# Performance work log

Measured on AMD Instinct MI355X. Metric: run time of the kernel, lower is better.

## Reference

```python
import jax, jax.numpy as jnp
import numpy as np
import math

D_MODEL = 1024
N_HEADS = 8
D_FF = 4 * D_MODEL
EPS = 1e-5


def layer_norm(x, g, b):
    mu = jnp.mean(x, axis=-1, keepdims=True)
    var = jnp.mean(jnp.square(x - mu), axis=-1, keepdims=True)
    return (x - mu) / jnp.sqrt(var + EPS) * g + b


def setup_inputs() -> dict:
    key = jax.random.key(0)
    ks = jax.random.split(key, 8)
    B, S = 1, 4096
    x = jax.random.normal(ks[0], (B, S, D_MODEL), dtype=jnp.float32)
    # linear params (stored as [in, out]); init scale ~ 1/sqrt(fan_in)
    qkv_w = jax.random.normal(ks[1], (D_MODEL, 3 * D_MODEL), dtype=jnp.float32) * (1.0 / math.sqrt(D_MODEL))
    qkv_b = jnp.zeros((3 * D_MODEL,), dtype=jnp.float32)
    w1 = jax.random.normal(ks[2], (D_MODEL, D_FF), dtype=jnp.float32) * (1.0 / math.sqrt(D_MODEL))
    b1 = jnp.zeros((D_FF,), dtype=jnp.float32)
    w2 = jax.random.normal(ks[3], (D_FF, D_MODEL), dtype=jnp.float32) * (1.0 / math.sqrt(D_FF))
    b2 = jnp.zeros((D_MODEL,), dtype=jnp.float32)
    ln1_g = jnp.ones((D_MODEL,), dtype=jnp.float32)
    ln1_b = jnp.zeros((D_MODEL,), dtype=jnp.float32)
    ln2_g = jnp.ones((D_MODEL,), dtype=jnp.float32)
    ln2_b = jnp.zeros((D_MODEL,), dtype=jnp.float32)
    return {"x": x, "ln1_g": ln1_g, "ln1_b": ln1_b, "qkv_w": qkv_w, "qkv_b": qkv_b,
            "ln2_g": ln2_g, "ln2_b": ln2_b, "w1": w1, "b1": b1, "w2": w2, "b2": b2}


def reference(x, ln1_g, ln1_b, qkv_w, qkv_b, ln2_g, ln2_b, w1, b1, w2, b2):
    B, S, D = x.shape
    hd = D // N_HEADS
    scaler = math.sqrt(hd)

    h = layer_norm(x, ln1_g, ln1_b)                       # [B,S,D]
    qkv = h @ qkv_w + qkv_b                               # [B,S,3D]
    q, k, v = jnp.split(qkv, 3, axis=-1)
    # b s (h d) -> b h s d
    def split_heads(t):
        return t.reshape(B, S, N_HEADS, hd).transpose(0, 2, 1, 3)
    q, k, v = split_heads(q), split_heads(k), split_heads(v)
    scores = jnp.einsum('bhqd,bhkd->bhqk', q, k) / scaler  # [B,H,S,S] materialized, as in source
    attn = jax.nn.softmax(scores, axis=-1)
    heads = jnp.einsum('bhqk,bhkd->bhqd', attn, v)        # [B,H,S,hd]
    attn_score = heads.transpose(0, 2, 1, 3).reshape(B, S, D)  # b h t d -> b t (h d)
    # NOTE: source returns attn_score (the proj Linear output is discarded)
    h = attn_score + h                                     # residual with ln1 output
    h = layer_norm(h, ln2_g, ln2_b)
    h = jax.nn.gelu(h @ w1 + b1, approximate=False) @ w2 + b2  # no final residual
    return h
```

## Files before the change

### kernel.cpp

```cpp
#include <hip/hip_runtime.h>
#include <stdint.h>


typedef __bf16 bf16;
typedef __attribute__((ext_vector_type(8))) __bf16 bf16x8;
typedef __attribute__((ext_vector_type(4))) __bf16 bf16x4;
typedef __attribute__((ext_vector_type(4))) float f32x4;

#define DEV static __device__ __forceinline__

#define QSCALE 0.12751741687f

DEV void gload_lds16(const void* gsrc, void* ldst) {
  typedef const __attribute__((address_space(1))) uint32_t gq_t;
  typedef __attribute__((address_space(3))) uint32_t lq_t;
  __builtin_amdgcn_global_load_lds((gq_t*)(uintptr_t)gsrc, (lq_t*)(uintptr_t)ldst,
                                   16, 0, 0);
}

DEV f32x4 mfma16(bf16x8 a, bf16x8 b, f32x4 c) {
  return __builtin_amdgcn_mfma_f32_16x16x32_bf16(a, b, c, 0, 0, 0);
}

__global__ __launch_bounds__(256) void ln1_kernel(
    const float* __restrict__ x, const float* __restrict__ gw,
    const float* __restrict__ bw, bf16* __restrict__ out) {
  int row = blockIdx.x, t = threadIdx.x;
  const float* xr = x + (size_t)row * 1024;
  f32x4 v = *(const f32x4*)(xr + t * 4);
  float s = v[0] + v[1] + v[2] + v[3];
  float s2 = v[0] * v[0] + v[1] * v[1] + v[2] * v[2] + v[3] * v[3];
#pragma unroll
  for (int off = 1; off < 64; off <<= 1) {
    s += __shfl_xor(s, off);
    s2 += __shfl_xor(s2, off);
  }
  __shared__ float red[8];
  if ((t & 63) == 0) { red[t >> 6] = s; red[4 + (t >> 6)] = s2; }
  __syncthreads();
  s = red[0] + red[1] + red[2] + red[3];
  s2 = red[4] + red[5] + red[6] + red[7];
  float mu = s * (1.f / 1024.f);
  float rstd = rsqrtf(s2 * (1.f / 1024.f) - mu * mu + 1e-5f);
  f32x4 gv = *(const f32x4*)(gw + t * 4);
  f32x4 bv = *(const f32x4*)(bw + t * 4);
  bf16x4 o;
#pragma unroll
  for (int j = 0; j < 4; j++) o[j] = (bf16)((v[j] - mu) * rstd * gv[j] + bv[j]);
  *(bf16x4*)(out + (size_t)row * 1024 + t * 4) = o;
}

__global__ __launch_bounds__(256) void resid_ln2_kernel(
    const bf16* __restrict__ Op, const float* __restrict__ lbuf,
    const bf16* __restrict__ h, const float* __restrict__ gw,
    const float* __restrict__ bw, bf16* __restrict__ out) {
  int row = blockIdx.x, t = threadIdx.x;
  int head = t >> 5;
  float l = 0.f;
  float acc[4] = {0.f, 0.f, 0.f, 0.f};
#pragma unroll
  for (int z = 0; z < 4; z++) {
    l += lbuf[(size_t)(z * 8 + head) * 4096 + row];
    bf16x4 ov = *(const bf16x4*)(Op + (size_t)z * 4096 * 1024 +
                                 (size_t)row * 1024 + t * 4);
#pragma unroll
    for (int j = 0; j < 4; j++) acc[j] += (float)ov[j];
  }
  float rl = 1.0f / l;
  bf16x4 hv = *(const bf16x4*)(h + (size_t)row * 1024 + t * 4);
  float vv[4];
#pragma unroll
  for (int j = 0; j < 4; j++) vv[j] = acc[j] * rl + (float)hv[j];
  float s = vv[0] + vv[1] + vv[2] + vv[3];
  float s2 = vv[0] * vv[0] + vv[1] * vv[1] + vv[2] * vv[2] + vv[3] * vv[3];
#pragma unroll
  for (int off = 1; off < 64; off <<= 1) {
    s += __shfl_xor(s, off);
    s2 += __shfl_xor(s2, off);
  }
  __shared__ float red[8];
  if ((t & 63) == 0) { red[t >> 6] = s; red[4 + (t >> 6)] = s2; }
  __syncthreads();
  s = red[0] + red[1] + red[2] + red[3];
  s2 = red[4] + red[5] + red[6] + red[7];
  float mu = s * (1.f / 1024.f);
  float rstd = rsqrtf(s2 * (1.f / 1024.f) - mu * mu + 1e-5f);
  f32x4 gv = *(const f32x4*)(gw + t * 4);
  f32x4 bv = *(const f32x4*)(bw + t * 4);
  bf16x4 o;
#pragma unroll
  for (int j = 0; j < 4; j++) o[j] = (bf16)((vv[j] - mu) * rstd * gv[j] + bv[j]);
  *(bf16x4*)(out + (size_t)row * 1024 + t * 4) = o;
}

__global__ __launch_bounds__(256) void transpose_f32_bf16(
    const float* __restrict__ in, bf16* __restrict__ out, int R, int C) {
  __shared__ float tile[32][33];
  int c0 = blockIdx.x * 32, r0 = blockIdx.y * 32;
  int tx = threadIdx.x & 31, ty = threadIdx.x >> 5;
#pragma unroll
  for (int j = 0; j < 4; j++)
    tile[ty + 8 * j][tx] = in[(size_t)(r0 + ty + 8 * j) * C + c0 + tx];
  __syncthreads();
#pragma unroll
  for (int j = 0; j < 4; j++)
    out[(size_t)(c0 + ty + 8 * j) * R + r0 + tx] = (bf16)tile[tx][ty + 8 * j];
}

template <int EPILOG>
__global__ __launch_bounds__(512) void gemm8_kernel(
    const bf16* __restrict__ A, const bf16* __restrict__ Bt,
    const float* __restrict__ bias, bf16* __restrict__ Cout,
    bf16* __restrict__ Vout, int M, int N, int K) {
  __shared__ bf16 sA[256 * 64];
  __shared__ bf16 sB[128 * 64];
  int nwg = gridDim.x * gridDim.y;
  int bid = blockIdx.y * gridDim.x + blockIdx.x;
  int swz = (bid & 7) * (nwg >> 3) + (bid >> 3);
  int bx = swz % gridDim.x, by = swz / gridDim.x;
  int m0 = by * 256, n0 = bx * 128;
  int tid = threadIdx.x;
  int wave = tid >> 6, lane = tid & 63;
  int lr = lane & 15, lg = lane >> 4;
  int wr = (wave >> 1) * 64, wc = (wave & 1) * 64;

  f32x4 acc[4][4] = {};

  int srow = tid >> 3;
  int scol = (tid & 7) * 8;
  const bf16* Abase = A + (size_t)(m0 + srow) * K + scol;
  const bf16* Bbase = Bt + (size_t)(n0 + srow) * K + scol;

  for (int kt = 0; kt < K; kt += 64) {
#pragma unroll
    for (int i = 0; i < 4; i++)
      gload_lds16(Abase + (size_t)(i * 64) * K + kt,
                  (char*)sA + i * 8192 + wave * 1024);
#pragma unroll
    for (int i = 0; i < 2; i++)
      gload_lds16(Bbase + (size_t)(i * 64) * K + kt,
                  (char*)sB + i * 8192 + wave * 1024);
    __syncthreads();
    bf16x8 af[4][2], bfv[4][2];
#pragma unroll
    for (int m = 0; m < 4; m++)
#pragma unroll
      for (int kk = 0; kk < 2; kk++)
        af[m][kk] = *(const bf16x8*)&sA[(wr + m * 16 + lr) * 64 + kk * 32 + lg * 8];
#pragma unroll
    for (int n = 0; n < 4; n++)
#pragma unroll
      for (int kk = 0; kk < 2; kk++)
        bfv[n][kk] = *(const bf16x8*)&sB[(wc + n * 16 + lr) * 64 + kk * 32 + lg * 8];
#pragma unroll
    for (int kk = 0; kk < 2; kk++)
#pragma unroll
      for (int m = 0; m < 4; m++)
#pragma unroll
        for (int n = 0; n < 4; n++)
          acc[m][n] = mfma16(af[m][kk], bfv[n][kk], acc[m][n]);
    __syncthreads();
  }

#pragma unroll
  for (int n = 0; n < 4; n++) {
    int col = n0 + wc + n * 16 + lr;
    float bs = bias[col];
#pragma unroll
    for (int m = 0; m < 4; m++) {
      int row0 = m0 + wr + m * 16 + lg * 4;
      if constexpr (EPILOG == 3) {
        if (col >= 2048) {
          bf16x4 pk;
#pragma unroll
          for (int r = 0; r < 4; r++) pk[r] = (bf16)(acc[m][n][r] + bs);
          *(bf16x4*)(Vout + (size_t)(col - 2048) * 4096 + row0) = pk;
          continue;
        }
      }
#pragma unroll
      for (int r = 0; r < 4; r++) {
        float v = acc[m][n][r] + bs;
        if constexpr (EPILOG == 1) {
          float u = v + 0.044715f * v * v * v;
          float e = __builtin_amdgcn_exp2f(-2.3021144f * u);
          v = v / (1.0f + e);
        }
        if constexpr (EPILOG == 3) { if (col < 1024) v *= QSCALE; }
        Cout[(size_t)(row0 + r) * N + col] = (bf16)v;
      }
    }
  }
}

__global__ __launch_bounds__(256) void gemm_ffn2_kernel(
    const bf16* __restrict__ A, const bf16* __restrict__ Bt,
    const float* __restrict__ bias, float* __restrict__ Cout,
    int M, int N, int K) {
  __shared__ bf16 sA[64 * 64];
  __shared__ bf16 sB[128 * 64];
  int nwg = gridDim.x * gridDim.y;
  int bid = blockIdx.y * gridDim.x + blockIdx.x;
  int swz = (bid & 7) * (nwg >> 3) + (bid >> 3);
  int bx = swz % gridDim.x, by = swz / gridDim.x;
  int m0 = by * 64, n0 = bx * 128;
  int tid = threadIdx.x;
  int wave = tid >> 6, lane = tid & 63;
  int lr = lane & 15, lg = lane >> 4;
  int wr = (wave >> 1) * 32, wc = (wave & 1) * 64;

  f32x4 acc[2][4] = {};

  int srow = tid >> 3;
  int scol = (tid & 7) * 8;
  const bf16* Abase = A + (size_t)(m0 + srow) * K + scol;
  const bf16* Bbase = Bt + (size_t)(n0 + srow) * K + scol;

  for (int kt = 0; kt < K; kt += 64) {
#pragma unroll
    for (int i = 0; i < 2; i++)
      gload_lds16(Abase + (size_t)(i * 32) * K + kt,
                  (char*)sA + i * 4096 + wave * 1024);
#pragma unroll
    for (int i = 0; i < 4; i++)
      gload_lds16(Bbase + (size_t)(i * 32) * K + kt,
                  (char*)sB + i * 4096 + wave * 1024);
    __syncthreads();
    bf16x8 af[2][2], bfv[4][2];
#pragma unroll
    for (int m = 0; m < 2; m++)
#pragma unroll
      for (int kk = 0; kk < 2; kk++)
        af[m][kk] = *(const bf16x8*)&sA[(wr + m * 16 + lr) * 64 + kk * 32 + lg * 8];
#pragma unroll
    for (int n = 0; n < 4; n++)
#pragma unroll
      for (int kk = 0; kk < 2; kk++)
        bfv[n][kk] = *(const bf16x8*)&sB[(wc + n * 16 + lr) * 64 + kk * 32 + lg * 8];
#pragma unroll
    for (int kk = 0; kk < 2; kk++)
#pragma unroll
      for (int m = 0; m < 2; m++)
#pragma unroll
        for (int n = 0; n < 4; n++)
          acc[m][n] = mfma16(af[m][kk], bfv[n][kk], acc[m][n]);
    __syncthreads();
  }

#pragma unroll
  for (int n = 0; n < 4; n++) {
    int col = n0 + wc + n * 16 + lr;
    float bs = bias[col];
#pragma unroll
    for (int m = 0; m < 2; m++) {
#pragma unroll
      for (int r = 0; r < 4; r++) {
        int row = m0 + wr + m * 16 + lg * 4 + r;
        Cout[(size_t)row * N + col] = acc[m][n][r] + bs;
      }
    }
  }
}

__global__ __launch_bounds__(256) void attn_kernel(
    const bf16* __restrict__ qkv, const bf16* __restrict__ vt,
    bf16* __restrict__ opart, float* __restrict__ lbuf) {
  constexpr int S = 4096, C3 = 3072;
  __shared__ bf16 sK[64 * 128];
  __shared__ bf16 sV[128 * 64];
  __shared__ bf16 sP[4 * 32 * 64];
  int hh = blockIdx.y;
  int q0 = blockIdx.x * 128;
  int z = blockIdx.z;
  int kv_begin = z * (S / 4), kv_end = kv_begin + (S / 4);
  bf16* obuf = opart + (size_t)z * 4096 * 1024;
  int tid = threadIdx.x, wave = tid >> 6, lane = tid & 63;
  int lr = lane & 15, lg = lane >> 4;

  bf16x8 qf[2][4];
#pragma unroll
  for (int qs = 0; qs < 2; qs++) {
    const bf16* qrow =
        qkv + (size_t)(q0 + wave * 32 + qs * 16 + lr) * C3 + hh * 128 + lg * 8;
#pragma unroll
    for (int kk = 0; kk < 4; kk++) qf[qs][kk] = *(const bf16x8*)(qrow + kk * 32);
  }
  f32x4 o[2][8] = {};
  float lsum[2] = {0.f, 0.f};

  const int krow_s = tid >> 4;
  const int kcb = (tid & 15) * 16;
  const int scbK = kcb ^ ((krow_s & 7) << 4);
  const int vrow_s = tid >> 3;
  const int vcb = (tid & 7) * 16;
  const int scbV = vcb ^ ((vrow_s & 7) << 4);

  const bf16* kbase = qkv + 1024 + hh * 128 + scbK / 2;
  const bf16* vbase = vt + (size_t)(hh * 128 + vrow_s) * S + scbV / 2;

  for (int kv0 = kv_begin; kv0 < kv_end; kv0 += 64) {
#pragma unroll
    for (int i = 0; i < 4; i++)
      gload_lds16(kbase + (size_t)(kv0 + i * 16 + krow_s) * C3,
                  (char*)sK + i * 4096 + wave * 1024);
#pragma unroll
    for (int i = 0; i < 4; i++)
      gload_lds16(vbase + (size_t)(i * 32) * S + kv0,
                  (char*)sV + i * 4096 + wave * 1024);
    __syncthreads();

    char* pw = (char*)sP + wave * 4096;

#pragma unroll
    for (int nf = 0; nf < 4; nf++) {
      f32x4 sc0 = {0.f, 0.f, 0.f, 0.f}, sc1 = sc0;
      __builtin_amdgcn_s_setprio(1);
#pragma unroll
      for (int kk = 0; kk < 4; kk++) {
        int krow = nf * 16 + lr;
        int db = (kk * 64 + lg * 16) ^ ((krow & 7) << 4);
        bf16x8 kf = *(const bf16x8*)((const char*)sK + krow * 256 + db);
        sc0 = mfma16(kf, qf[0][kk], sc0);
        sc1 = mfma16(kf, qf[1][kk], sc1);
      }
      __builtin_amdgcn_s_setprio(0);
      f32x4 scs[2] = {sc0, sc1};
#pragma unroll
      for (int qs = 0; qs < 2; qs++) {
        float p0 = __builtin_amdgcn_exp2f(scs[qs][0]);
        float p1 = __builtin_amdgcn_exp2f(scs[qs][1]);
        float p2 = __builtin_amdgcn_exp2f(scs[qs][2]);
        float p3 = __builtin_amdgcn_exp2f(scs[qs][3]);
        lsum[qs] += (p0 + p1) + (p2 + p3);
        bf16x4 pk;
        pk[0] = (bf16)p0; pk[1] = (bf16)p1; pk[2] = (bf16)p2; pk[3] = (bf16)p3;
        *(bf16x4*)(pw + (qs * 16 + lr) * 128 +
                   ((nf * 32 + lg * 8) ^ ((lr & 7) << 4))) = pk;
      }
    }

    bf16x8 pa[2][2];
#pragma unroll
    for (int qs = 0; qs < 2; qs++)
#pragma unroll
      for (int kk = 0; kk < 2; kk++) {
        int db = (kk * 64 + lg * 16) ^ ((lr & 7) << 4);
        pa[qs][kk] = *(const bf16x8*)(pw + (qs * 16 + lr) * 128 + db);
      }
    __builtin_amdgcn_s_setprio(1);
#pragma unroll
    for (int df = 0; df < 8; df++) {
#pragma unroll
      for (int kk = 0; kk < 2; kk++) {
        int vrow = df * 16 + lr;
        int db = (kk * 64 + lg * 16) ^ ((vrow & 7) << 4);
        bf16x8 vf = *(const bf16x8*)((const char*)sV + vrow * 128 + db);
        o[0][df] = mfma16(pa[0][kk], vf, o[0][df]);
        o[1][df] = mfma16(pa[1][kk], vf, o[1][df]);
      }
    }
    __builtin_amdgcn_s_setprio(0);
    __syncthreads();
  }

#pragma unroll
  for (int qs = 0; qs < 2; qs++) {
    float ls = lsum[qs];
    ls += __shfl_xor(ls, 16);
    ls += __shfl_xor(ls, 32);
    if (lg == 0)
      lbuf[(size_t)(z * 8 + hh) * 4096 + q0 + wave * 32 + qs * 16 + lr] = ls;
#pragma unroll
    for (int df = 0; df < 8; df++) {
      int col = hh * 128 + df * 16 + lr;
#pragma unroll
      for (int r = 0; r < 4; r++) {
        int row = q0 + wave * 32 + qs * 16 + lg * 4 + r;
        obuf[(size_t)row * 1024 + col] = (bf16)o[qs][df][r];
      }
    }
  }
}

extern "C" void kernel_launch(void* const* d_in, const int* in_sizes, int n_in,
                              void* d_out, int out_size, void* d_ws, size_t ws_size,
                              hipStream_t stream) {
  const float* x     = (const float*)d_in[0];
  const float* ln1_g = (const float*)d_in[1];
  const float* ln1_b = (const float*)d_in[2];
  const float* qkv_w = (const float*)d_in[3];
  const float* qkv_b = (const float*)d_in[4];
  const float* ln2_g = (const float*)d_in[5];
  const float* ln2_b = (const float*)d_in[6];
  const float* w1    = (const float*)d_in[7];
  const float* b1    = (const float*)d_in[8];
  const float* w2    = (const float*)d_in[9];
  const float* b2    = (const float*)d_in[10];

  char* ws = (char*)d_ws;
  const size_t MB = 1ull << 20;
  bf16*  h    = (bf16*)(ws + 0);
  bf16*  qkv  = (bf16*)(ws + 8 * MB);
  bf16*  h2   = (bf16*)(ws + 8 * MB);
  bf16*  w1T  = (bf16*)(ws + 16 * MB);
  bf16*  w2T  = (bf16*)(ws + 24 * MB);
  bf16*  vt   = (bf16*)(ws + 32 * MB);
  bf16*  Op   = (bf16*)(ws + 40 * MB);
  bf16*  ffn1 = (bf16*)(ws + 40 * MB);
  float* lbuf = (float*)(ws + 72 * MB);
  bf16*  wTq  = (bf16*)(ws + 72 * MB + 512 * 1024);
  float* outp = (float*)d_out;

  ln1_kernel<<<4096, 256, 0, stream>>>(x, ln1_g, ln1_b, h);
  transpose_f32_bf16<<<dim3(3072 / 32, 1024 / 32), 256, 0, stream>>>(qkv_w, wTq, 1024, 3072);
  gemm8_kernel<3><<<dim3(3072 / 128, 4096 / 256), 512, 0, stream>>>(
      h, wTq, qkv_b, qkv, vt, 4096, 3072, 1024);
  attn_kernel<<<dim3(32, 8, 4), 256, 0, stream>>>(qkv, vt, Op, lbuf);
  transpose_f32_bf16<<<dim3(4096 / 32, 1024 / 32), 256, 0, stream>>>(w1, w1T, 1024, 4096);
  transpose_f32_bf16<<<dim3(1024 / 32, 4096 / 32), 256, 0, stream>>>(w2, w2T, 4096, 1024);
  resid_ln2_kernel<<<4096, 256, 0, stream>>>(Op, lbuf, h, ln2_g, ln2_b, h2);
  gemm8_kernel<1><<<dim3(4096 / 128, 4096 / 256), 512, 0, stream>>>(
      h2, w1T, b1, ffn1, nullptr, 4096, 4096, 1024);
  gemm_ffn2_kernel<<<dim3(1024 / 128, 4096 / 64), 256, 0, stream>>>(
      ffn1, w2T, b2, outp, 4096, 1024, 4096);
}
```

Before: 277.3 us.

## Rewrite QKV/FFN1 GEMM as 256x256 double-buffered pipelined kernel with swizzled LDS

Replaces the 256x128 single-buffered GEMM with a 256x256 tile kernel that double-buffers A and B in 128KB of dynamic LDS. It interleaves quarter-tile async loads with MFMA quadrants using fine-grained barriers and vmcnt waits, and uses XOR-swizzled LDS addressing to avoid bank conflicts. The aim is to hide global load latency behind compute and raise arithmetic intensity per block. In exchange, the grid gets fewer, larger blocks (192 for QKV, 256 for FFN1) and each block holds 128 accumulator registers per lane, which may hurt occupancy and load balance across 256 CUs.

```diff
diff --git a/kernel.cpp b/kernel.cpp
--- a/kernel.cpp
+++ b/kernel.cpp
@@ -108,58 +108,112 @@
 }
 
 template <int EPILOG>
-__global__ __launch_bounds__(512) void gemm8_kernel(
+__global__ __launch_bounds__(512) void gemm8p_kernel(
     const bf16* __restrict__ A, const bf16* __restrict__ Bt,
     const float* __restrict__ bias, bf16* __restrict__ Cout,
     bf16* __restrict__ Vout, int M, int N, int K) {
-  __shared__ bf16 sA[256 * 64];
-  __shared__ bf16 sB[128 * 64];
+  extern __shared__ char smem[];
   int nwg = gridDim.x * gridDim.y;
   int bid = blockIdx.y * gridDim.x + blockIdx.x;
   int swz = (bid & 7) * (nwg >> 3) + (bid >> 3);
   int bx = swz % gridDim.x, by = swz / gridDim.x;
-  int m0 = by * 256, n0 = bx * 128;
-  int tid = threadIdx.x;
-  int wave = tid >> 6, lane = tid & 63;
+  int m0 = by * 256, n0 = bx * 256;
+  int tid = threadIdx.x, wave = tid >> 6, lane = tid & 63;
   int lr = lane & 15, lg = lane >> 4;
-  int wr = (wave >> 1) * 64, wc = (wave & 1) * 64;
-
-  f32x4 acc[4][4] = {};
-
-  int srow = tid >> 3;
-  int scol = (tid & 7) * 8;
-  const bf16* Abase = A + (size_t)(m0 + srow) * K + scol;
-  const bf16* Bbase = Bt + (size_t)(n0 + srow) * K + scol;
-
-  for (int kt = 0; kt < K; kt += 64) {
-#pragma unroll
-    for (int i = 0; i < 4; i++)
-      gload_lds16(Abase + (size_t)(i * 64) * K + kt,
-                  (char*)sA + i * 8192 + wave * 1024);
-#pragma unroll
-    for (int i = 0; i < 2; i++)
-      gload_lds16(Bbase + (size_t)(i * 64) * K + kt,
-                  (char*)sB + i * 8192 + wave * 1024);
-    __syncthreads();
-    bf16x8 af[4][2], bfv[4][2];
-#pragma unroll
-    for (int m = 0; m < 4; m++)
-#pragma unroll
-      for (int kk = 0; kk < 2; kk++)
-        af[m][kk] = *(const bf16x8*)&sA[(wr + m * 16 + lr) * 64 + kk * 32 + lg * 8];
-#pragma unroll
-    for (int n = 0; n < 4; n++)
-#pragma unroll
-      for (int kk = 0; kk < 2; kk++)
-        bfv[n][kk] = *(const bf16x8*)&sB[(wc + n * 16 + lr) * 64 + kk * 32 + lg * 8];
+  int wr = (wave >> 2) * 128;
+  int wc = (wave & 3) * 64;
+  const int NT = K >> 6;
+
+  f32x4 acc[8][4] = {};
+
+  const int sArow = tid >> 3;
+  const int scbA = ((tid & 7) * 16) ^ (((tid >> 3) & 7) << 4);
+  const int scbB = ((lane & 7) * 16) ^ ((lane >> 3) << 4);
+
+  auto stageA = [&](int c, int T) {
+    char* sAb = smem + (size_t)(T & 1) * 32768;
+#pragma unroll
+    for (int j = 0; j < 2; j++) {
+      int r0 = j * 128 + 64 * c;
+      gload_lds16(A + (size_t)(m0 + r0 + sArow) * K + T * 64 + scbA / 2,
+                  sAb + r0 * 128 + wave * 1024);
+    }
+  };
+  auto stageB = [&](int c, int T) {
+    char* sBb = smem + 65536 + (size_t)(T & 1) * 32768;
+    int wrun = (wave >> 2) * 64 + 32 * c + (wave & 3) * 8;
+#pragma unroll
+    for (int j = 0; j < 2; j++) {
+      int r0 = j * 128 + wrun;
+      gload_lds16(Bt + (size_t)(n0 + r0 + (lane >> 3)) * K + T * 64 + scbB / 2,
+                  sBb + r0 * 128);
+    }
+  };
+  auto ldA = [&](bf16x8 (&af)[4][2], int qm, int b) {
+    const char* sAb = smem + (size_t)b * 32768;
+#pragma unroll
+    for (int mm = 0; mm < 4; mm++)
+#pragma unroll
+      for (int kk = 0; kk < 2; kk++) {
+        int rl = wr + 64 * qm + mm * 16 + lr;
+        int db = (kk * 64 + lg * 16) ^ ((rl & 7) << 4);
+        af[mm][kk] = *(const bf16x8*)(sAb + rl * 128 + db);
+      }
+  };
+  auto ldB = [&](bf16x8 (&bfv)[2][2], int qn, int b) {
+    const char* sBb = smem + 65536 + (size_t)b * 32768;
+#pragma unroll
+    for (int nn = 0; nn < 2; nn++)
+#pragma unroll
+      for (int kk = 0; kk < 2; kk++) {
+        int rb = wc + 32 * qn + nn * 16 + lr;
+        int db = (kk * 64 + lg * 16) ^ ((rb & 7) << 4);
+        bfv[nn][kk] = *(const bf16x8*)(sBb + rb * 128 + db);
+      }
+  };
+  auto mfmaQ = [&](bf16x8 (&af)[4][2], bf16x8 (&bfv)[2][2], int qm, int qn) {
+    __builtin_amdgcn_s_setprio(1);
 #pragma unroll
     for (int kk = 0; kk < 2; kk++)
 #pragma unroll
-      for (int m = 0; m < 4; m++)
-#pragma unroll
-        for (int n = 0; n < 4; n++)
-          acc[m][n] = mfma16(af[m][kk], bfv[n][kk], acc[m][n]);
-    __syncthreads();
+      for (int mm = 0; mm < 4; mm++)
+#pragma unroll
+        for (int nn = 0; nn < 2; nn++)
+          acc[qm * 4 + mm][qn * 2 + nn] =
+              mfma16(af[mm][kk], bfv[nn][kk], acc[qm * 4 + mm][qn * 2 + nn]);
+    __builtin_amdgcn_s_setprio(0);
+  };
+
+  stageA(0, 0); stageB(0, 0); stageA(1, 0); stageB(1, 0);
+  stageA(0, 1); stageB(0, 1);
+  asm volatile("s_waitcnt vmcnt(4)" ::: "memory");
+  __builtin_amdgcn_s_barrier();
+
+  for (int T = 0; T < NT; T++) {
+    int b = T & 1;
+    bf16x8 af[4][2], bfv[2][2];
+    ldA(af, 0, b); ldB(bfv, 0, b);
+    if (T + 1 < NT) stageA(1, T + 1);
+    __builtin_amdgcn_s_barrier();
+    mfmaQ(af, bfv, 0, 0);
+    __builtin_amdgcn_s_barrier();
+    ldB(bfv, 1, b);
+    if (T + 1 < NT) stageB(1, T + 1);
+    __builtin_amdgcn_s_barrier();
+    mfmaQ(af, bfv, 0, 1);
+    __builtin_amdgcn_s_barrier();
+    ldA(af, 1, b); ldB(bfv, 0, b);
+    if (T + 2 < NT) stageA(0, T + 2);
+    __builtin_amdgcn_s_barrier();
+    mfmaQ(af, bfv, 1, 0);
+    __builtin_amdgcn_s_barrier();
+    ldB(bfv, 1, b);
+    if (T + 2 < NT) stageB(0, T + 2);
+    __builtin_amdgcn_s_barrier();
+    mfmaQ(af, bfv, 1, 1);
+    if (T < NT - 2) asm volatile("s_waitcnt vmcnt(4)" ::: "memory");
+    else            asm volatile("s_waitcnt vmcnt(0)" ::: "memory");
+    __builtin_amdgcn_s_barrier();
   }
 
 #pragma unroll
@@ -167,7 +221,7 @@
     int col = n0 + wc + n * 16 + lr;
     float bs = bias[col];
 #pragma unroll
-    for (int m = 0; m < 4; m++) {
+    for (int m = 0; m < 8; m++) {
       int row0 = m0 + wr + m * 16 + lg * 4;
       if constexpr (EPILOG == 3) {
         if (col >= 2048) {
@@ -411,15 +465,20 @@
   bf16*  wTq  = (bf16*)(ws + 72 * MB + 512 * 1024);
   float* outp = (float*)d_out;
 
+  hipFuncSetAttribute(reinterpret_cast<const void*>(gemm8p_kernel<3>),
+                      hipFuncAttributeMaxDynamicSharedMemorySize, 131072);
+  hipFuncSetAttribute(reinterpret_cast<const void*>(gemm8p_kernel<1>),
+                      hipFuncAttributeMaxDynamicSharedMemorySize, 131072);
+
   ln1_kernel<<<4096, 256, 0, stream>>>(x, ln1_g, ln1_b, h);
   transpose_f32_bf16<<<dim3(3072 / 32, 1024 / 32), 256, 0, stream>>>(qkv_w, wTq, 1024, 3072);
-  gemm8_kernel<3><<<dim3(3072 / 128, 4096 / 256), 512, 0, stream>>>(
+  gemm8p_kernel<3><<<dim3(3072 / 256, 4096 / 256), 512, 131072, stream>>>(
       h, wTq, qkv_b, qkv, vt, 4096, 3072, 1024);
   attn_kernel<<<dim3(32, 8, 4), 256, 0, stream>>>(qkv, vt, Op, lbuf);
   transpose_f32_bf16<<<dim3(4096 / 32, 1024 / 32), 256, 0, stream>>>(w1, w1T, 1024, 4096);
   transpose_f32_bf16<<<dim3(1024 / 32, 4096 / 32), 256, 0, stream>>>(w2, w2T, 4096, 1024);
   resid_ln2_kernel<<<4096, 256, 0, stream>>>(Op, lbuf, h, ln2_g, ln2_b, h2);
-  gemm8_kernel<1><<<dim3(4096 / 128, 4096 / 256), 512, 0, stream>>>(
+  gemm8p_kernel<1><<<dim3(4096 / 256, 4096 / 256), 512, 131072, stream>>>(
       h2, w1T, b1, ffn1, nullptr, 4096, 4096, 1024);
   gemm_ffn2_kernel<<<dim3(1024 / 128, 4096 / 64), 256, 0, stream>>>(
       ffn1, w2T, b2, outp, 4096, 1024, 4096);
```

Measured after the change: 266.6 us. -3.9%, faster.
